# Kernel optimization log

Measured on AMD Instinct MI355X. Metric: run time of the kernel, lower is better.

## Reference

```python
import jax, jax.numpy as jnp
import numpy as np

H = 128   # hidden_size
NL = 3    # num_layers
R = 32    # water_rows (Water2sea_slice_num)
O = 48    # water_cols (Original_slice_len)
B = 64    # batch_size
F = 32    # input_size
L = R + O - 1  # Water2sea_slice_len (wavefront length)


def setup_inputs():
    key = jax.random.key(0)
    k1, k2, k3, k4 = jax.random.split(key, 4)
    stdv = 1.0 / np.sqrt(H)
    inp = jax.random.normal(k1, (B, R, O, F), dtype=jnp.float32)
    W_first = jax.random.uniform(k2, (6 * H, F + 2 * H), minval=-stdv, maxval=stdv, dtype=jnp.float32)
    W_other = jax.random.uniform(k3, (NL - 1, 6 * H, 4 * H), minval=-stdv, maxval=stdv, dtype=jnp.float32)
    Bias = jax.random.uniform(k4, (NL, 6 * H), minval=-stdv, maxval=stdv, dtype=jnp.float32)
    return {"input": inp, "W_first": W_first, "W_other": W_other, "Bias": Bias,
            "batch_size": B, "input_size": F, "flag": 0}


def _forward(inp, W_first, W_other, Bias, batch_size, input_size, flag):
    # permute: flag==0 -> [rows, batch, cols, feat]
    x = jnp.transpose(inp, (2, 0, 1, 3)) if flag == 1 else jnp.transpose(inp, (1, 0, 2, 3))
    Rn, bs, On, Fn = x.shape
    Ln = Rn + On - 1
    # wavefront-shifted input: row r occupies slices [r, r+On) (input_transfer)
    padded = jnp.pad(x, ((0, 0), (0, 0), (0, Rn - 1), (0, 0)))                 # [R,B,L,F]
    shifted = jax.vmap(lambda t, r: jnp.roll(t, r, axis=1))(padded, jnp.arange(Rn))
    a0 = shifted.reshape(Rn * bs, Ln, Fn)
    # bias applied to row-group g at slice s iff (s < Rn) and (g <= s)  [faithful to linear()]
    s_idx = jnp.arange(Ln)[:, None]
    g_idx = jnp.arange(Rn)[None, :]
    bias_mask = ((g_idx <= s_idx) & (s_idx < Rn)).astype(jnp.float32)          # [L,R]
    bias_mask = jnp.repeat(bias_mask, bs, axis=1)[..., None]                   # [L,RB,1]

    def run_layer(a, W, bvec):
        # a: [RB, L, feat]; W: [6H, feat+2H]; bvec: [6H]
        def step(carry, xs):
            h_row, h_col = carry
            a_s, m_s = xs
            z = jnp.concatenate([h_row, h_col, a_s], axis=-1)
            gate = z @ W.T + m_s * bvec                                        # [RB,6H]
            sig = jax.nn.sigmoid(gate[:, :4 * H])
            tnh = jnp.tanh(gate[:, 4 * H:])
            ur, orow, uc, ocol = jnp.split(sig, 4, axis=-1)
            ir, ic = jnp.split(tnh, 2, axis=-1)
            h_row_n = jnp.tanh((1.0 - ur) * h_row + ur * ir) * orow
            h_col_n = jnp.tanh((1.0 - uc) * h_col + uc * ic) * ocol
            out = jnp.concatenate([h_row_n, h_col_n], axis=-1)
            h_col_roll = jnp.roll(h_col_n, bs, axis=0)  # transfer col hidden to next row
            return (h_row_n, h_col_roll), (out, h_row_n, h_col_n)
        h0 = jnp.zeros((Rn * bs, H), a.dtype)
        _, (outs, hrows, hcols) = jax.lax.scan(step, (h0, h0), (jnp.swapaxes(a, 0, 1), bias_mask))
        return outs, hrows, hcols  # each [L, RB, *]

    row_saves, col_saves = [], []
    a = a0
    for layer in range(NL):
        W = W_first if layer == 0 else W_other[layer - 1]
        outs, hrows, hcols = run_layer(a, W, Bias[layer])
        hrows = hrows.reshape(Ln, Rn, bs, H)
        hcols = hcols.reshape(Ln, Rn, bs, H)
        # row r finishes at slice On-1+r; col hidden of last row-group saved for slices >= Rn-1
        row_saves.append(hrows[On - 1 + jnp.arange(Rn), jnp.arange(Rn)])       # [R,B,H]
        col_saves.append(hcols[Rn - 1:, Rn - 1])                               # [O,B,H]
        a = jnp.swapaxes(outs, 0, 1)                                           # [RB,L,2H]; dropout p=0 -> identity
    output_all_slice = a
    hidden_row_all = jnp.transpose(jnp.stack(row_saves), (2, 0, 1, 3))         # [B,NL,R,H]
    hidden_col_all = jnp.transpose(jnp.stack(col_saves), (2, 0, 1, 3))         # [B,NL,O,H]
    return output_all_slice, hidden_row_all, hidden_col_all


def reference(input, W_first, W_other, Bias, batch_size, input_size, flag):
    return _forward(input, W_first, W_other, Bias, batch_size, input_size, flag)
```

## Files before the change

### kernel.cpp

```cpp
#include <hip/hip_runtime.h>
#include <stdint.h>

#define HH   128
#define NLAY 3
#define RR   32
#define OO   48
#define BBX  64
#define FFX  32
#define LLX  (RR + OO - 1)
#define RBr  (RR * BBX)
#define N6   (6 * HH)
#define TSTEPS (LLX + NLAY - 1)
#define NBLOCKS 192

typedef unsigned short u16;
typedef __attribute__((ext_vector_type(8))) short short8;
typedef __attribute__((ext_vector_type(4))) float f32x4;

#define OFF_ABUF0 ((size_t)0)
#define SZ_ABUF0  ((size_t)LLX * RBr * FFX * 2)
#define OFF_HZ    (OFF_ABUF0 + SZ_ABUF0)
#define SZ_HZ     ((size_t)NLAY * 2 * RBr * 256 * 2)
#define OFF_BAR   (OFF_HZ + SZ_HZ)
#define SZ_BAR    ((size_t)32768)
#define SZ_STATE  (SZ_HZ + SZ_BAR)

__device__ __forceinline__ u16 f2b(float x) {
  uint32_t u = __float_as_uint(x);
  return (u16)((u + 0x7FFFu + ((u >> 16) & 1u)) >> 16);
}
__device__ __forceinline__ float rcp_(float x) { return __builtin_amdgcn_rcpf(x); }
__device__ __forceinline__ float sigmoidf_(float x) {
  return rcp_(1.0f + __expf(-x));
}
__device__ __forceinline__ float tanhf_(float x) {
  return 1.0f - 2.0f * rcp_(__expf(2.0f * x) + 1.0f);
}

__global__ __launch_bounds__(256) void k_prep_input(const float* __restrict__ inp,
                                                    u16* __restrict__ abuf0) {
  int idx = blockIdx.x * 256 + threadIdx.x;
  if (idx >= LLX * RBr * FFX) return;
  int f   = idx & (FFX - 1);
  int row = (idx >> 5) & (RBr - 1);
  int s   = idx / (RBr * FFX);
  int g = row >> 6, b = row & 63;
  int o = s - g;
  float v = (o >= 0 && o < OO) ? inp[((b * RR + g) * OO + o) * FFX + f] : 0.0f;
  abuf0[idx] = f2b(v);
}

__global__ __launch_bounds__(256) void k_zero(uint32_t* __restrict__ p, size_t nwords) {
  size_t i = (size_t)blockIdx.x * 256 + threadIdx.x;
  size_t stride = (size_t)gridDim.x * 256;
  for (; i < nwords; i += stride) p[i] = 0u;
}

template <int KK>
__device__ __forceinline__ void stage_w(const float* __restrict__ Wsrc, int jblk,
                                        u16* __restrict__ Wl) {
  constexpr int NFRAG = (KK / 32) * 6;
  for (int e = threadIdx.x; e < NFRAG * 64; e += 512) {
    int kcm = e >> 6, ln = e & 63;
    int kc = kcm / 6, m = kcm - kc * 6;
    int fr2 = ln & 15, hi2 = ln >> 4;
    int srow = m * 128 + jblk * 16 + fr2;
    const float* src = Wsrc + (size_t)srow * KK + kc * 32 + hi2 * 8;
    short8 v;
#pragma unroll
    for (int x = 0; x < 8; ++x) v[x] = (short)f2b(src[x]);
    *(short8*)&Wl[(size_t)e * 8] = v;
  }
}

template <int KK>
__device__ __forceinline__ void persist_body(char* __restrict__ ws,
                                             const float* __restrict__ Bias_l,
                                             float* __restrict__ out,
                                             int layer, int jblk, int bblk, bool light,
                                             u16* __restrict__ Wl,
                                             float* __restrict__ hcl,
                                             uint32_t* __restrict__ arrC,
                                             uint32_t* __restrict__ epoC,
                                             bool leader) {
  constexpr int NCH = KK / 32;
  constexpr int RD  = 3;
  const int tid = threadIdx.x;
  const int lane = tid & 63, w = tid >> 6;
  const int fr = lane & 15, hi = lane >> 4;
  const int myslot = layer * 8 + jblk;

  const int bcol = bblk * 8 + (fr & 7);
  const int g00   = w * 4 + (fr >> 3);
  const int arow0 = g00 * 64 + bcol;
  const int arp0  = ((g00 + 1) & 31) * 64 + bcol;
  const int g01   = g00 + 2;
  const int arow1 = g01 * 64 + bcol;
  const int arp1  = ((g01 + 1) & 31) * 64 + bcol;
  const int j = jblk * 16 + fr;
  const u16* wfrag = &Wl[lane * 8];
  float bia[6];
#pragma unroll
  for (int m = 0; m < 6; ++m) bia[m] = Bias_l[m * 128 + j];

  u16*   hz_base  = (u16*)(ws + OFF_HZ) + (size_t)layer * 2 * RBr * 256;
  u16*   hzp_base = (u16*)(ws + OFF_HZ) + (size_t)(layer - 1) * 2 * RBr * 256;
  u16*   abuf0    = (u16*)(ws + OFF_ABUF0);
  float* hid_row  = out + (size_t)RBr * LLX * 256;
  float* hid_col  = hid_row + (size_t)BBX * NLAY * RR * HH;

  float hr_reg[2][4];
#pragma unroll
  for (int t2 = 0; t2 < 2; ++t2)
#pragma unroll
    for (int q = 0; q < 4; ++q) hr_reg[t2][q] = 0.0f;

  for (int t = 0; t < TSTEPS; ++t) {
    const int s = t - layer;
    const uint32_t target = (uint32_t)(t + 1);
    float sv_r[2][4], sv_c[2][4];
#pragma unroll
    for (int t2 = 0; t2 < 2; ++t2)
#pragma unroll
      for (int q = 0; q < 4; ++q) { sv_r[t2][q] = 0.0f; sv_c[t2][q] = 0.0f; }

    if (s >= 0 && s < LLX) {
      const int sW = s & 1, sR = sW ^ 1;
      const u16* hzR = hz_base + (size_t)sR * RBr * 256;
      u16*       hzW = hz_base + (size_t)sW * RBr * 256;
      const u16* hzP = hzp_base + (size_t)sW * RBr * 256;
      const u16* ab_s = abuf0 + (size_t)s * RBr * FFX;
      const float* hcR = hcl + sR * 4352;
      float*       hcW = hcl + sW * 4352;

      if (w * 4 <= s) {
        auto LDK = [&](int ar, int ap, int kc) -> short8 {
          if (kc < 8)
            return *(const short8*)&hzR[ar * 256 + kc * 32 + hi * 8];
          if constexpr (KK == 288) {
            return *(const short8*)&ab_s[ar * FFX + hi * 8];
          } else {
            if (kc < 12)
              return *(const short8*)&hzP[ar * 256 + (kc - 8) * 32 + hi * 8];
            return *(const short8*)&hzP[ap * 256 + 128 + (kc - 12) * 32 + hi * 8];
          }
        };

        f32x4 z4 = {0.f, 0.f, 0.f, 0.f};
        f32x4 acc0[6], acc1[6];
#pragma unroll
        for (int m = 0; m < 6; ++m) { acc0[m] = z4; acc1[m] = z4; }

        short8 ring0[RD], ring1[RD];
#pragma unroll
        for (int i = 0; i < RD; ++i) {
          ring0[i] = LDK(arow0, arp0, i);
          ring1[i] = LDK(arow1, arp1, i);
        }
        __builtin_amdgcn_s_setprio(1);
#pragma unroll
        for (int kc = 0; kc < NCH; ++kc) {
          short8 a0 = ring0[kc % RD];
          short8 a1 = ring1[kc % RD];
          if (kc + RD < NCH) {
            ring0[kc % RD] = LDK(arow0, arp0, kc + RD);
            ring1[kc % RD] = LDK(arow1, arp1, kc + RD);
          }
#pragma unroll
          for (int m = 0; m < 6; ++m) {
            short8 bv = *(const short8*)&wfrag[(size_t)(kc * 6 + m) * 512];
            acc0[m] = __builtin_amdgcn_mfma_f32_16x16x32_bf16(a0, bv, acc0[m], 0, 0, 0);
            acc1[m] = __builtin_amdgcn_mfma_f32_16x16x32_bf16(a1, bv, acc1[m], 0, 0, 0);
          }
        }
        __builtin_amdgcn_s_setprio(0);

#pragma unroll
        for (int t2 = 0; t2 < 2; ++t2) {
          const int g = w * 4 + 2 * t2 + (hi >> 1);
          const int gp = (g + 1) & (RR - 1);
          const float msk = (g <= s && s < RR) ? 1.0f : 0.0f;
          float mb[6];
#pragma unroll
          for (int m = 0; m < 6; ++m) mb[m] = msk * bia[m];
#pragma unroll
          for (int q = 0; q < 4; ++q) {
            const f32x4* A = t2 ? acc1 : acc0;
            const int lb = (hi & 1) * 4 + q;
            const int b  = bblk * 8 + lb;
            const int row = g * 64 + b;
            const int lrow = g * 8 + lb;
            const int rp = gp * 64 + b;
            const int lrp = gp * 8 + lb;
            float ur  = sigmoidf_(A[0][q] + mb[0]);
            float orw = sigmoidf_(A[1][q] + mb[1]);
            float uc  = sigmoidf_(A[2][q] + mb[2]);
            float oc  = sigmoidf_(A[3][q] + mb[3]);
            float ir  = tanhf_(A[4][q] + mb[4]);
            float ic  = tanhf_(A[5][q] + mb[5]);
            float hr_o = hr_reg[t2][q];
            float hc_o = hcR[lrow * 17 + fr];
            float hr_n = tanhf_((1.0f - ur) * hr_o + ur * ir) * orw;
            float hc_n = tanhf_((1.0f - uc) * hc_o + uc * ic) * oc;
            hr_reg[t2][q] = hr_n;
            sv_r[t2][q] = hr_n;
            sv_c[t2][q] = hc_n;
            hcW[lrp * 17 + fr] = hc_n;
            hzW[row * 256 + j] = f2b(hr_n);
            hzW[rp * 256 + HH + j] = f2b(hc_n);
          }
        }
      } else {
#pragma unroll
        for (int t2 = 0; t2 < 2; ++t2) {
          const int g = w * 4 + 2 * t2 + (hi >> 1);
          const int gp = (g + 1) & (RR - 1);
#pragma unroll
          for (int q = 0; q < 4; ++q) {
            const int lb = (hi & 1) * 4 + q;
            const int b  = bblk * 8 + lb;
            const int row = g * 64 + b;
            const int rp = gp * 64 + b;
            const int lrp = gp * 8 + lb;
            hcW[lrp * 17 + fr] = 0.0f;
            hzW[row * 256 + j] = 0;
            hzW[rp * 256 + HH + j] = 0;
          }
        }
      }
    }

    __syncthreads();
    if (tid == 0) {
      if (!light) __threadfence();
      __hip_atomic_store(&arrC[myslot * 16], target, __ATOMIC_RELAXED,
                         __HIP_MEMORY_SCOPE_AGENT);
    }

    if (s >= 0 && s < LLX) {
#pragma unroll
      for (int t2 = 0; t2 < 2; ++t2) {
        const int g = w * 4 + 2 * t2 + (hi >> 1);
#pragma unroll
        for (int q = 0; q < 4; ++q) {
          const int lb = (hi & 1) * 4 + q;
          const int b  = bblk * 8 + lb;
          const int row = g * 64 + b;
          if (layer == 2) {
            out[((size_t)row * LLX + s) * 256 + j] = sv_r[t2][q];
            out[((size_t)row * LLX + s) * 256 + HH + j] = sv_c[t2][q];
          }
          if (s - g == OO - 1)
            hid_row[((size_t)(b * NLAY + layer) * RR + g) * HH + j] = sv_r[t2][q];
          if (g == RR - 1 && s >= RR - 1)
            hid_col[((size_t)(b * NLAY + layer) * OO + (s - (RR - 1))) * HH + j] = sv_c[t2][q];
        }
      }
    }

    if (leader) {
      if (tid < 24) {
        while (__hip_atomic_load(&arrC[tid * 16], __ATOMIC_RELAXED,
                                 __HIP_MEMORY_SCOPE_AGENT) < target)
          __builtin_amdgcn_s_sleep(1);
      }
      __syncthreads();
      if (tid == 0)
        __hip_atomic_store(epoC, target, __ATOMIC_RELAXED, __HIP_MEMORY_SCOPE_AGENT);
    }
    if (tid == 0) {
      while (__hip_atomic_load(epoC, __ATOMIC_RELAXED, __HIP_MEMORY_SCOPE_AGENT) < target)
        __builtin_amdgcn_s_sleep(1);
      if (!light) __threadfence();
    }
    __syncthreads();
    if (light) asm volatile("buffer_inv" ::: "memory");
  }
}

__global__ __launch_bounds__(512) void k_persist(char* __restrict__ ws,
                                                 const float* __restrict__ Wf,
                                                 const float* __restrict__ Wo,
                                                 const float* __restrict__ Bias,
                                                 float* __restrict__ out) {
  __shared__ u16 Wl[49152];
  __shared__ float hcl[8704];
  __shared__ uint32_t sh_light;
  const int bx = blockIdx.x;
  const int layer = bx >> 6, jblk = (bx >> 3) & 7, bblk = bx & 7;
  const int tid = threadIdx.x;

  if (layer == 0) stage_w<288>(Wf, jblk, Wl);
  else            stage_w<512>(Wo + (size_t)(layer - 1) * N6 * 512, jblk, Wl);
  for (int e = tid; e < 8704; e += 512) hcl[e] = 0.0f;

  uint32_t xcc;
  asm volatile("s_getreg_b32 %0, hwreg(20, 0, 4)" : "=s"(xcc));
  uint32_t* barG  = (uint32_t*)(ws + OFF_BAR);
  uint32_t* table = (uint32_t*)(ws + OFF_BAR + 256);
  uint32_t* arrC  = (uint32_t*)(ws + OFF_BAR + 4096 + (size_t)bblk * 2048);
  uint32_t* epoC  = (uint32_t*)(ws + OFF_BAR + 24576 + (size_t)bblk * 256);
  const bool leader = (layer == 0 && jblk == 0);
  __syncthreads();
  if (tid == 0) {
    __hip_atomic_store(&table[bx], xcc, __ATOMIC_RELAXED, __HIP_MEMORY_SCOPE_AGENT);
    __hip_atomic_fetch_add(barG, 1u, __ATOMIC_RELEASE, __HIP_MEMORY_SCOPE_AGENT);
    while (__hip_atomic_load(barG, __ATOMIC_ACQUIRE, __HIP_MEMORY_SCOPE_AGENT) < NBLOCKS)
      __builtin_amdgcn_s_sleep(1);
    uint32_t lt = 1u;
    for (int q2 = 0; q2 < 24; ++q2) {
      uint32_t v = __hip_atomic_load(&table[q2 * 8 + bblk], __ATOMIC_RELAXED,
                                     __HIP_MEMORY_SCOPE_AGENT);
      lt &= (v == xcc) ? 1u : 0u;
    }
    sh_light = lt;
  }
  __syncthreads();
  const bool light = (sh_light != 0u);

  const float* bias_l = Bias + layer * N6;
  if (layer == 0)
    persist_body<288>(ws, bias_l, out, 0, jblk, bblk, light, Wl, hcl,
                      arrC, epoC, leader);
  else
    persist_body<512>(ws, bias_l, out, layer, jblk, bblk, light, Wl, hcl,
                      arrC, epoC, leader);
}

extern "C" void kernel_launch(void* const* d_in, const int* in_sizes, int n_in,
                              void* d_out, int out_size, void* d_ws, size_t ws_size,
                              hipStream_t stream) {
  const float* inp  = (const float*)d_in[0];
  const float* Wf   = (const float*)d_in[1];
  const float* Wo   = (const float*)d_in[2];
  const float* Bias = (const float*)d_in[3];
  float* out = (float*)d_out;
  char* ws = (char*)d_ws;
  (void)in_sizes; (void)n_in; (void)out_size; (void)ws_size;

  k_prep_input<<<(LLX * RBr * FFX) / 256, 256, 0, stream>>>(inp, (u16*)(ws + OFF_ABUF0));
  k_zero<<<2048, 256, 0, stream>>>((uint32_t*)(ws + OFF_HZ), SZ_STATE / 4);
  k_persist<<<NBLOCKS, 512, 0, stream>>>(ws, Wf, Wo, Bias, out);
}
```

Baseline: 789.1 us.

## Split row and column gate work across two wave halves in 1024-thread blocks

Doubles the persistent block to 1024 threads. The low 8 waves compute the row-direction gates (ur, orow, ir) and the high 8 waves compute the column-direction gates (uc, ocol, ic). Each wave now issues half as many MFMAs per step, and its accumulator and register footprint shrinks, so the serial per-step critical path should get shorter. The cost is that the A-operand loads are duplicated across both halves, more waves take part in each block barrier, and register pressure under launch_bounds(1024) is tighter.

```diff
diff --git a/kernel.cpp b/kernel.cpp
--- a/kernel.cpp
+++ b/kernel.cpp
@@ -60,7 +60,7 @@
 __device__ __forceinline__ void stage_w(const float* __restrict__ Wsrc, int jblk,
                                         u16* __restrict__ Wl) {
   constexpr int NFRAG = (KK / 32) * 6;
-  for (int e = threadIdx.x; e < NFRAG * 64; e += 512) {
+  for (int e = threadIdx.x; e < NFRAG * 64; e += 1024) {
     int kcm = e >> 6, ln = e & 63;
     int kc = kcm / 6, m = kcm - kc * 6;
     int fr2 = ln & 15, hi2 = ln >> 4;
@@ -87,21 +87,26 @@
   constexpr int RD  = 3;
   const int tid = threadIdx.x;
   const int lane = tid & 63, w = tid >> 6;
+  const int wq = w & 7;
+  const bool low = (w < 8);
   const int fr = lane & 15, hi = lane >> 4;
   const int myslot = layer * 8 + jblk;
 
   const int bcol = bblk * 8 + (fr & 7);
-  const int g00   = w * 4 + (fr >> 3);
+  const int g00   = wq * 4 + (fr >> 3);
   const int arow0 = g00 * 64 + bcol;
   const int arp0  = ((g00 + 1) & 31) * 64 + bcol;
-  const int g01   = g00 + 2;
-  const int arow1 = g01 * 64 + bcol;
-  const int arp1  = ((g01 + 1) & 31) * 64 + bcol;
+  const int arow1 = (g00 + 2) * 64 + bcol;
+  const int arp1  = ((g00 + 3) & 31) * 64 + bcol;
   const int j = jblk * 16 + fr;
   const u16* wfrag = &Wl[lane * 8];
-  float bia[6];
-#pragma unroll
-  for (int m = 0; m < 6; ++m) bia[m] = Bias_l[m * 128 + j];
+  const u16* wA = wfrag + (size_t)(low ? 0 : 2) * 512;
+  const u16* wB = wfrag + (size_t)(low ? 1 : 3) * 512;
+  const u16* wC = wfrag + (size_t)(low ? 4 : 5) * 512;
+  float bia[3];
+  bia[0] = Bias_l[(low ? 0 : 2) * 128 + j];
+  bia[1] = Bias_l[(low ? 1 : 3) * 128 + j];
+  bia[2] = Bias_l[(low ? 4 : 5) * 128 + j];
 
   u16*   hz_base  = (u16*)(ws + OFF_HZ) + (size_t)layer * 2 * RBr * 256;
   u16*   hzp_base = (u16*)(ws + OFF_HZ) + (size_t)(layer - 1) * 2 * RBr * 256;
@@ -118,11 +123,11 @@
   for (int t = 0; t < TSTEPS; ++t) {
     const int s = t - layer;
     const uint32_t target = (uint32_t)(t + 1);
-    float sv_r[2][4], sv_c[2][4];
+    float sv[2][4];
 #pragma unroll
     for (int t2 = 0; t2 < 2; ++t2)
 #pragma unroll
-      for (int q = 0; q < 4; ++q) { sv_r[t2][q] = 0.0f; sv_c[t2][q] = 0.0f; }
+      for (int q = 0; q < 4; ++q) sv[t2][q] = 0.0f;
 
     if (s >= 0 && s < LLX) {
       const int sW = s & 1, sR = sW ^ 1;
@@ -133,7 +138,7 @@
       const float* hcR = hcl + sR * 4352;
       float*       hcW = hcl + sW * 4352;
 
-      if (w * 4 <= s) {
+      if (wq * 4 <= s) {
         auto LDK = [&](int ar, int ap, int kc) -> short8 {
           if (kc < 8)
             return *(const short8*)&hzR[ar * 256 + kc * 32 + hi * 8];
@@ -147,9 +152,9 @@
         };
 
         f32x4 z4 = {0.f, 0.f, 0.f, 0.f};
-        f32x4 acc0[6], acc1[6];
-#pragma unroll
-        for (int m = 0; m < 6; ++m) { acc0[m] = z4; acc1[m] = z4; }
+        f32x4 acc0[3], acc1[3];
+#pragma unroll
+        for (int m = 0; m < 3; ++m) { acc0[m] = z4; acc1[m] = z4; }
 
         short8 ring0[RD], ring1[RD];
 #pragma unroll
@@ -166,65 +171,72 @@
             ring0[kc % RD] = LDK(arow0, arp0, kc + RD);
             ring1[kc % RD] = LDK(arow1, arp1, kc + RD);
           }
-#pragma unroll
-          for (int m = 0; m < 6; ++m) {
-            short8 bv = *(const short8*)&wfrag[(size_t)(kc * 6 + m) * 512];
-            acc0[m] = __builtin_amdgcn_mfma_f32_16x16x32_bf16(a0, bv, acc0[m], 0, 0, 0);
-            acc1[m] = __builtin_amdgcn_mfma_f32_16x16x32_bf16(a1, bv, acc1[m], 0, 0, 0);
-          }
+          short8 bvA = *(const short8*)&wA[(size_t)kc * 3072];
+          short8 bvB = *(const short8*)&wB[(size_t)kc * 3072];
+          short8 bvC = *(const short8*)&wC[(size_t)kc * 3072];
+          acc0[0] = __builtin_amdgcn_mfma_f32_16x16x32_bf16(a0, bvA, acc0[0], 0, 0, 0);
+          acc1[0] = __builtin_amdgcn_mfma_f32_16x16x32_bf16(a1, bvA, acc1[0], 0, 0, 0);
+          acc0[1] = __builtin_amdgcn_mfma_f32_16x16x32_bf16(a0, bvB, acc0[1], 0, 0, 0);
+          acc1[1] = __builtin_amdgcn_mfma_f32_16x16x32_bf16(a1, bvB, acc1[1], 0, 0, 0);
+          acc0[2] = __builtin_amdgcn_mfma_f32_16x16x32_bf16(a0, bvC, acc0[2], 0, 0, 0);
+          acc1[2] = __builtin_amdgcn_mfma_f32_16x16x32_bf16(a1, bvC, acc1[2], 0, 0, 0);
         }
         __builtin_amdgcn_s_setprio(0);
 
 #pragma unroll
         for (int t2 = 0; t2 < 2; ++t2) {
-          const int g = w * 4 + 2 * t2 + (hi >> 1);
+          const f32x4* A = t2 ? acc1 : acc0;
+          const int g = wq * 4 + 2 * t2 + (hi >> 1);
           const int gp = (g + 1) & (RR - 1);
           const float msk = (g <= s && s < RR) ? 1.0f : 0.0f;
-          float mb[6];
-#pragma unroll
-          for (int m = 0; m < 6; ++m) mb[m] = msk * bia[m];
-#pragma unroll
-          for (int q = 0; q < 4; ++q) {
-            const f32x4* A = t2 ? acc1 : acc0;
-            const int lb = (hi & 1) * 4 + q;
-            const int b  = bblk * 8 + lb;
-            const int row = g * 64 + b;
-            const int lrow = g * 8 + lb;
-            const int rp = gp * 64 + b;
-            const int lrp = gp * 8 + lb;
-            float ur  = sigmoidf_(A[0][q] + mb[0]);
-            float orw = sigmoidf_(A[1][q] + mb[1]);
-            float uc  = sigmoidf_(A[2][q] + mb[2]);
-            float oc  = sigmoidf_(A[3][q] + mb[3]);
-            float ir  = tanhf_(A[4][q] + mb[4]);
-            float ic  = tanhf_(A[5][q] + mb[5]);
-            float hr_o = hr_reg[t2][q];
-            float hc_o = hcR[lrow * 17 + fr];
-            float hr_n = tanhf_((1.0f - ur) * hr_o + ur * ir) * orw;
-            float hc_n = tanhf_((1.0f - uc) * hc_o + uc * ic) * oc;
-            hr_reg[t2][q] = hr_n;
-            sv_r[t2][q] = hr_n;
-            sv_c[t2][q] = hc_n;
-            hcW[lrp * 17 + fr] = hc_n;
-            hzW[row * 256 + j] = f2b(hr_n);
-            hzW[rp * 256 + HH + j] = f2b(hc_n);
-          }
-        }
-      } else {
-#pragma unroll
-        for (int t2 = 0; t2 < 2; ++t2) {
-          const int g = w * 4 + 2 * t2 + (hi >> 1);
-          const int gp = (g + 1) & (RR - 1);
+          float mb[3];
+#pragma unroll
+          for (int m = 0; m < 3; ++m) mb[m] = msk * bia[m];
 #pragma unroll
           for (int q = 0; q < 4; ++q) {
             const int lb = (hi & 1) * 4 + q;
             const int b  = bblk * 8 + lb;
             const int row = g * 64 + b;
-            const int rp = gp * 64 + b;
-            const int lrp = gp * 8 + lb;
-            hcW[lrp * 17 + fr] = 0.0f;
-            hzW[row * 256 + j] = 0;
-            hzW[rp * 256 + HH + j] = 0;
+            if (low) {
+              float ur  = sigmoidf_(A[0][q] + mb[0]);
+              float orw = sigmoidf_(A[1][q] + mb[1]);
+              float ir  = tanhf_(A[2][q] + mb[2]);
+              float hr_n = tanhf_((1.0f - ur) * hr_reg[t2][q] + ur * ir) * orw;
+              hr_reg[t2][q] = hr_n;
+              sv[t2][q] = hr_n;
+              hzW[row * 256 + j] = f2b(hr_n);
+            } else {
+              const int lrow = g * 8 + lb;
+              const int rp = gp * 64 + b;
+              const int lrp = gp * 8 + lb;
+              float uc = sigmoidf_(A[0][q] + mb[0]);
+              float oc = sigmoidf_(A[1][q] + mb[1]);
+              float ic = tanhf_(A[2][q] + mb[2]);
+              float hc_n = tanhf_((1.0f - uc) * hcR[lrow * 17 + fr] + uc * ic) * oc;
+              sv[t2][q] = hc_n;
+              hcW[lrp * 17 + fr] = hc_n;
+              hzW[rp * 256 + HH + j] = f2b(hc_n);
+            }
+          }
+        }
+      } else {
+#pragma unroll
+        for (int t2 = 0; t2 < 2; ++t2) {
+          const int g = wq * 4 + 2 * t2 + (hi >> 1);
+          const int gp = (g + 1) & (RR - 1);
+#pragma unroll
+          for (int q = 0; q < 4; ++q) {
+            const int lb = (hi & 1) * 4 + q;
+            const int b  = bblk * 8 + lb;
+            const int row = g * 64 + b;
+            if (low) {
+              hzW[row * 256 + j] = 0;
+            } else {
+              const int rp = gp * 64 + b;
+              const int lrp = gp * 8 + lb;
+              hcW[lrp * 17 + fr] = 0.0f;
+              hzW[rp * 256 + HH + j] = 0;
+            }
           }
         }
       }
@@ -240,20 +252,23 @@
     if (s >= 0 && s < LLX) {
 #pragma unroll
       for (int t2 = 0; t2 < 2; ++t2) {
-        const int g = w * 4 + 2 * t2 + (hi >> 1);
+        const int g = wq * 4 + 2 * t2 + (hi >> 1);
 #pragma unroll
         for (int q = 0; q < 4; ++q) {
           const int lb = (hi & 1) * 4 + q;
           const int b  = bblk * 8 + lb;
           const int row = g * 64 + b;
-          if (layer == 2) {
-            out[((size_t)row * LLX + s) * 256 + j] = sv_r[t2][q];
-            out[((size_t)row * LLX + s) * 256 + HH + j] = sv_c[t2][q];
-          }
-          if (s - g == OO - 1)
-            hid_row[((size_t)(b * NLAY + layer) * RR + g) * HH + j] = sv_r[t2][q];
-          if (g == RR - 1 && s >= RR - 1)
-            hid_col[((size_t)(b * NLAY + layer) * OO + (s - (RR - 1))) * HH + j] = sv_c[t2][q];
+          if (low) {
+            if (layer == 2)
+              out[((size_t)row * LLX + s) * 256 + j] = sv[t2][q];
+            if (s - g == OO - 1)
+              hid_row[((size_t)(b * NLAY + layer) * RR + g) * HH + j] = sv[t2][q];
+          } else {
+            if (layer == 2)
+              out[((size_t)row * LLX + s) * 256 + HH + j] = sv[t2][q];
+            if (g == RR - 1 && s >= RR - 1)
+              hid_col[((size_t)(b * NLAY + layer) * OO + (s - (RR - 1))) * HH + j] = sv[t2][q];
+          }
         }
       }
     }
@@ -278,11 +293,11 @@
   }
 }
 
-__global__ __launch_bounds__(512) void k_persist(char* __restrict__ ws,
-                                                 const float* __restrict__ Wf,
-                                                 const float* __restrict__ Wo,
-                                                 const float* __restrict__ Bias,
-                                                 float* __restrict__ out) {
+__global__ __launch_bounds__(1024, 4) void k_persist(char* __restrict__ ws,
+                                                     const float* __restrict__ Wf,
+                                                     const float* __restrict__ Wo,
+                                                     const float* __restrict__ Bias,
+                                                     float* __restrict__ out) {
   __shared__ u16 Wl[49152];
   __shared__ float hcl[8704];
   __shared__ uint32_t sh_light;
@@ -292,7 +307,7 @@
 
   if (layer == 0) stage_w<288>(Wf, jblk, Wl);
   else            stage_w<512>(Wo + (size_t)(layer - 1) * N6 * 512, jblk, Wl);
-  for (int e = tid; e < 8704; e += 512) hcl[e] = 0.0f;
+  for (int e = tid; e < 8704; e += 1024) hcl[e] = 0.0f;
 
   uint32_t xcc;
   asm volatile("s_getreg_b32 %0, hwreg(20, 0, 4)" : "=s"(xcc));
@@ -340,5 +355,5 @@
 
   k_prep_input<<<(LLX * RBr * FFX) / 256, 256, 0, stream>>>(inp, (u16*)(ws + OFF_ABUF0));
   k_zero<<<2048, 256, 0, stream>>>((uint32_t*)(ws + OFF_HZ), SZ_STATE / 4);
-  k_persist<<<NBLOCKS, 512, 0, stream>>>(ws, Wf, Wo, Bias, out);
-}
+  k_persist<<<NBLOCKS, 1024, 0, stream>>>(ws, Wf, Wo, Bias, out);
+}
```

Result: slower. 1.345 ms (+70.5%).
